# Optimization experiments

Hardware: AMD Instinct MI355X
Metric: run time of the kernel (lower is better)

Reference implementation:

```python
import jax, jax.numpy as jnp
import numpy as np

B, C, H = 64, 64, 32

def _pm_cross_pairs(ks):
    # Replicates PM_cross(2, ks): pairs (i, i+j) ordered by gap j=1..ks-1, then i.
    a, b = [], []
    for j in range(1, ks):
        for i in range(ks - j):
            a.append(i)
            b.append(i + j)
    return np.array(a, dtype=np.int32), np.array(b, dtype=np.int32)

def setup_inputs() -> dict:
    key = jax.random.key(0)
    k1, k2 = jax.random.split(key)
    ia, ib = _pm_cross_pairs(H)           # 496 pairs for H=32
    hk = ia.shape[0] + 2 * H              # 560
    x = jax.random.normal(k1, (B, C, H, H), dtype=jnp.float32)
    weight = 0.1 * jax.random.normal(k2, (C, H, hk, H), dtype=jnp.float32)
    return {"x": x, "weight": weight, "idx_a": jnp.asarray(ia), "idx_b": jnp.asarray(ib)}

def reference(x, weight, idx_a, idx_b):
    # cross-term products along last axis: [B,C,H,P]
    cross = x[..., idx_a] * x[..., idx_b]
    feat = jnp.concatenate([x, x * x, cross], axis=-1)  # [B,C,H,Hk]
    # per-(channel,row) grouped matmul
    return jnp.einsum('bcij,cijo->bcio', feat, weight)
```

## Files before the change

kernel.cpp:

```cpp
#include <hip/hip_runtime.h>

#define NB 64
#define NC 64
#define NH 32
#define HK 560
#define NOCT 88
#define NCHUNK 11
#define XSTR 50

typedef __bf16 bf16x8 __attribute__((ext_vector_type(8)));
typedef float f32x4 __attribute__((ext_vector_type(4)));

__global__ __launch_bounds__(256, 4) void hconv_kernel(
    const float* __restrict__ x, const float* __restrict__ w,
    const int* __restrict__ idx_a, const int* __restrict__ idx_b,
    float* __restrict__ out)
{
    __shared__ float s_x[NB * XSTR];
    __shared__ unsigned s_desc[NOCT];
    __shared__ __align__(16) unsigned short s_wT[2][32][72];

    const int t = threadIdx.x;
    const int g = blockIdx.x;
    const int c = g >> 5, i = g & 31;

    {
        const int xrow = t >> 2, seg = t & 3;
        const float* xr = x + (((size_t)xrow * NC + c) * NH + i) * NH + seg * 8;
        float4 v0 = *(const float4*)(xr);
        float4 v1 = *(const float4*)(xr + 4);
        float* dst = &s_x[xrow * XSTR + seg * 8];
        dst[0] = v0.x; dst[1] = v0.y; dst[2] = v0.z; dst[3] = v0.w;
        dst[4] = v1.x; dst[5] = v1.y; dst[6] = v1.z; dst[7] = v1.w;
        if (seg == 0) {
            #pragma unroll
            for (int m = 0; m < 8; ++m) {
                s_x[xrow * XSTR + 32 + m] = 0.0f;
                s_x[xrow * XSTR + 40 + m] = 1.0f;
            }
        }
    }

    if (t < NOCT) {
        unsigned pa, pb, ko, val;
        if (t < 4)      { pa = 8u * t; pb = 40u; ko = 8u * t; val = 8u; }
        else if (t < 8) { unsigned u = t - 4; pa = pb = 8u * u; ko = 32u + 8u * u; val = 8u; }
        else if (t < 84) {
            unsigned q = t - 8, j, a;
            if (q < 28)      { j = 1 + q / 4;        a = q % 4; }
            else if (q < 52) { j = 8 + (q - 28) / 3; a = (q - 28) % 3; }
            else if (q < 68) { j = 16 + (q - 52) / 2; a = (q - 52) % 2; }
            else             { j = 24 + (q - 68);     a = 0; }
            unsigned r = 32 - j;
            pa = 8 * a; pb = 8 * a + j;
            unsigned rem = r - 8 * a;
            val = rem < 8u ? rem : 8u;
            ko = 64u + (j - 1) * 32u - (j * (j - 1)) / 2u + 8u * a;
        } else { pa = 40u; pb = 40u; ko = 0u; val = 0u; }
        s_desc[t] = pa | (pb << 6) | (ko << 12) | (val << 22);
    }

    const int wv = t >> 6;
    const int lane = t & 63;
    const int lr = lane & 15;
    const int lq = lane >> 4;
    const int arow = wv * 16 + lr;
    const int wo = t & 31;
    const int wkg = t >> 5;

    const float* wbase = w + (size_t)(c * NH + i) * HK * NH;

    __syncthreads();

    {
        const unsigned d = s_desc[wkg];
        const unsigned ko = (d >> 12) & 0x3ffu, val = d >> 22;
        bf16x8 wv8;
        #pragma unroll
        for (int r = 0; r < 8; ++r) {
            float v = (r < (int)val)
                ? __builtin_nontemporal_load(&wbase[(size_t)(ko + r) * NH + wo]) : 0.0f;
            wv8[r] = (__bf16)v;
        }
        *(bf16x8*)&s_wT[0][wo][wkg * 8] = wv8;
    }
    __syncthreads();

    f32x4 acc0 = {0.f, 0.f, 0.f, 0.f};
    f32x4 acc1 = {0.f, 0.f, 0.f, 0.f};

    for (int ch = 0; ch < NCHUNK; ++ch) {
        const int buf = ch & 1;

        float pv[8];
        if (ch + 1 < NCHUNK) {
            const unsigned d = s_desc[(ch + 1) * 8 + wkg];
            const unsigned ko = (d >> 12) & 0x3ffu, val = d >> 22;
            #pragma unroll
            for (int r = 0; r < 8; ++r)
                pv[r] = (r < (int)val)
                    ? __builtin_nontemporal_load(&wbase[(size_t)(ko + r) * NH + wo]) : 0.0f;
        }

        #pragma unroll
        for (int ks = 0; ks < 2; ++ks) {
            const unsigned d = s_desc[ch * 8 + ks * 4 + lq];
            const float* pA = &s_x[arow * XSTR + (d & 63u)];
            const float* pB = &s_x[arow * XSTR + ((d >> 6) & 63u)];
            bf16x8 a;
            #pragma unroll
            for (int j2 = 0; j2 < 8; ++j2)
                a[j2] = (__bf16)(pA[j2] * pB[j2]);
            bf16x8 b0 = *(const bf16x8*)&s_wT[buf][lr][ks * 32 + lq * 8];
            bf16x8 b1 = *(const bf16x8*)&s_wT[buf][16 + lr][ks * 32 + lq * 8];
            acc0 = __builtin_amdgcn_mfma_f32_16x16x32_bf16(a, b0, acc0, 0, 0, 0);
            acc1 = __builtin_amdgcn_mfma_f32_16x16x32_bf16(a, b1, acc1, 0, 0, 0);
        }

        if (ch + 1 < NCHUNK) {
            bf16x8 wv8;
            #pragma unroll
            for (int r = 0; r < 8; ++r) wv8[r] = (__bf16)pv[r];
            *(bf16x8*)&s_wT[buf ^ 1][wo][wkg * 8] = wv8;
        }
        __syncthreads();
    }

    #pragma unroll
    for (int r = 0; r < 4; ++r) {
        const int b = wv * 16 + lq * 4 + r;
        float* op = out + (((size_t)b * NC + c) * NH + i) * NH;
        op[lr] = acc0[r];
        op[16 + lr] = acc1[r];
    }
}

extern "C" void kernel_launch(void* const* d_in, const int* in_sizes, int n_in,
                              void* d_out, int out_size, void* d_ws, size_t ws_size,
                              hipStream_t stream) {
    const float* x = (const float*)d_in[0];
    const float* w = (const float*)d_in[1];
    const int* idx_a = (const int*)d_in[2];
    const int* idx_b = (const int*)d_in[3];
    float* out = (float*)d_out;
    hconv_kernel<<<dim3(NC * NH), dim3(256), 0, stream>>>(x, w, idx_a, idx_b, out);
}
```

Measured before the change: 278.6 us.

## Load weights directly into registers per wave, dropping LDS staging and barriers

Removes the shared-memory weight staging buffer and its per-chunk __syncthreads. Each wave now loads its B-fragment weights straight from global memory into registers and converts them to bf16. Partial final octets are handled by clamping ko to 552 and shifting the x offsets, with zero padding in a wider x row (stride 57), so the per-row valid-count masking is no longer needed. This raises the occupancy hint to 5 blocks per CU. The trade-off is that the four waves each load the same weights redundantly, relying on the cache, and the loads no longer use nontemporal hints.

```diff
diff --git a/kernel.cpp b/kernel.cpp
--- a/kernel.cpp
+++ b/kernel.cpp
@@ -6,19 +6,18 @@
 #define HK 560
 #define NOCT 88
 #define NCHUNK 11
-#define XSTR 50
+#define XSTR 57
 
 typedef __bf16 bf16x8 __attribute__((ext_vector_type(8)));
 typedef float f32x4 __attribute__((ext_vector_type(4)));
 
-__global__ __launch_bounds__(256, 4) void hconv_kernel(
+__global__ __launch_bounds__(256, 5) void hconv_kernel(
     const float* __restrict__ x, const float* __restrict__ w,
     const int* __restrict__ idx_a, const int* __restrict__ idx_b,
     float* __restrict__ out)
 {
     __shared__ float s_x[NB * XSTR];
     __shared__ unsigned s_desc[NOCT];
-    __shared__ __align__(16) unsigned short s_wT[2][32][72];
 
     const int t = threadIdx.x;
     const int g = blockIdx.x;
@@ -29,101 +28,93 @@
         const float* xr = x + (((size_t)xrow * NC + c) * NH + i) * NH + seg * 8;
         float4 v0 = *(const float4*)(xr);
         float4 v1 = *(const float4*)(xr + 4);
-        float* dst = &s_x[xrow * XSTR + seg * 8];
+        float* dst = &s_x[xrow * XSTR + 8 + seg * 8];
         dst[0] = v0.x; dst[1] = v0.y; dst[2] = v0.z; dst[3] = v0.w;
         dst[4] = v1.x; dst[5] = v1.y; dst[6] = v1.z; dst[7] = v1.w;
         if (seg == 0) {
+            float* r0 = &s_x[xrow * XSTR];
             #pragma unroll
             for (int m = 0; m < 8; ++m) {
-                s_x[xrow * XSTR + 32 + m] = 0.0f;
-                s_x[xrow * XSTR + 40 + m] = 1.0f;
+                r0[m] = 0.0f;
+                r0[40 + m] = 0.0f;
+                r0[48 + m] = 1.0f;
             }
         }
     }
 
     if (t < NOCT) {
-        unsigned pa, pb, ko, val;
-        if (t < 4)      { pa = 8u * t; pb = 40u; ko = 8u * t; val = 8u; }
-        else if (t < 8) { unsigned u = t - 4; pa = pb = 8u * u; ko = 32u + 8u * u; val = 8u; }
+        unsigned pa, pb, ko;
+        if (t < 4)      { pa = 8u + 8u * t; pb = 48u; ko = 8u * t; }
+        else if (t < 8) { unsigned u = t - 4; pa = pb = 8u + 8u * u; ko = 32u + 8u * u; }
         else if (t < 84) {
             unsigned q = t - 8, j, a;
-            if (q < 28)      { j = 1 + q / 4;        a = q % 4; }
-            else if (q < 52) { j = 8 + (q - 28) / 3; a = (q - 28) % 3; }
+            if (q < 28)      { j = 1 + q / 4;         a = q % 4; }
+            else if (q < 52) { j = 8 + (q - 28) / 3;  a = (q - 28) % 3; }
             else if (q < 68) { j = 16 + (q - 52) / 2; a = (q - 52) % 2; }
             else             { j = 24 + (q - 68);     a = 0; }
-            unsigned r = 32 - j;
-            pa = 8 * a; pb = 8 * a + j;
-            unsigned rem = r - 8 * a;
-            val = rem < 8u ? rem : 8u;
             ko = 64u + (j - 1) * 32u - (j * (j - 1)) / 2u + 8u * a;
-        } else { pa = 40u; pb = 40u; ko = 0u; val = 0u; }
-        s_desc[t] = pa | (pb << 6) | (ko << 12) | (val << 22);
+            pa = 8u + 8u * a; pb = pa + j;
+            if (ko > 552u) { unsigned s = ko - 552u; ko = 552u; pa -= s; pb -= s; }
+        } else { pa = 0u; pb = 0u; ko = 0u; }
+        s_desc[t] = pa | (pb << 6) | (ko << 12);
     }
 
-    const int wv = t >> 6;
-    const int lane = t & 63;
-    const int lr = lane & 15;
-    const int lq = lane >> 4;
+    const int wv = t >> 6, lane = t & 63;
+    const int lr = lane & 15, lq = lane >> 4;
     const int arow = wv * 16 + lr;
-    const int wo = t & 31;
-    const int wkg = t >> 5;
+    const float* wbase = w + (size_t)(c * NH + i) * HK * NH;
+    const float* xrp = &s_x[arow * XSTR];
 
-    const float* wbase = w + (size_t)(c * NH + i) * HK * NH;
-
-    __syncthreads();
-
-    {
-        const unsigned d = s_desc[wkg];
-        const unsigned ko = (d >> 12) & 0x3ffu, val = d >> 22;
-        bf16x8 wv8;
-        #pragma unroll
-        for (int r = 0; r < 8; ++r) {
-            float v = (r < (int)val)
-                ? __builtin_nontemporal_load(&wbase[(size_t)(ko + r) * NH + wo]) : 0.0f;
-            wv8[r] = (__bf16)v;
-        }
-        *(bf16x8*)&s_wT[0][wo][wkg * 8] = wv8;
-    }
     __syncthreads();
 
     f32x4 acc0 = {0.f, 0.f, 0.f, 0.f};
     f32x4 acc1 = {0.f, 0.f, 0.f, 0.f};
 
+    unsigned d0 = s_desc[lq];
+    unsigned d1 = s_desc[4 + lq];
+
     for (int ch = 0; ch < NCHUNK; ++ch) {
-        const int buf = ch & 1;
+        unsigned nd0 = 0, nd1 = 0;
+        if (ch + 1 < NCHUNK) {
+            nd0 = s_desc[(ch + 1) * 8 + lq];
+            nd1 = s_desc[(ch + 1) * 8 + 4 + lq];
+        }
+        const unsigned pa0 = d0 & 63u, pb0 = (d0 >> 6) & 63u, ko0 = d0 >> 12;
+        const unsigned pa1 = d1 & 63u, pb1 = (d1 >> 6) & 63u, ko1 = d1 >> 12;
 
-        float pv[8];
-        if (ch + 1 < NCHUNK) {
-            const unsigned d = s_desc[(ch + 1) * 8 + wkg];
-            const unsigned ko = (d >> 12) & 0x3ffu, val = d >> 22;
-            #pragma unroll
-            for (int r = 0; r < 8; ++r)
-                pv[r] = (r < (int)val)
-                    ? __builtin_nontemporal_load(&wbase[(size_t)(ko + r) * NH + wo]) : 0.0f;
+        const float* wb0 = wbase + (size_t)ko0 * NH + lr;
+        const float* wb1 = wbase + (size_t)ko1 * NH + lr;
+        float b0v[8], b1v[8], b2v[8], b3v[8];
+        #pragma unroll
+        for (int j = 0; j < 8; ++j) {
+            b0v[j] = wb0[j * NH];
+            b1v[j] = wb0[j * NH + 16];
+            b2v[j] = wb1[j * NH];
+            b3v[j] = wb1[j * NH + 16];
         }
 
+        const float* pA0 = xrp + pa0; const float* pB0 = xrp + pb0;
+        const float* pA1 = xrp + pa1; const float* pB1 = xrp + pb1;
+        bf16x8 a0, a1;
         #pragma unroll
-        for (int ks = 0; ks < 2; ++ks) {
-            const unsigned d = s_desc[ch * 8 + ks * 4 + lq];
-            const float* pA = &s_x[arow * XSTR + (d & 63u)];
-            const float* pB = &s_x[arow * XSTR + ((d >> 6) & 63u)];
-            bf16x8 a;
-            #pragma unroll
-            for (int j2 = 0; j2 < 8; ++j2)
-                a[j2] = (__bf16)(pA[j2] * pB[j2]);
-            bf16x8 b0 = *(const bf16x8*)&s_wT[buf][lr][ks * 32 + lq * 8];
-            bf16x8 b1 = *(const bf16x8*)&s_wT[buf][16 + lr][ks * 32 + lq * 8];
-            acc0 = __builtin_amdgcn_mfma_f32_16x16x32_bf16(a, b0, acc0, 0, 0, 0);
-            acc1 = __builtin_amdgcn_mfma_f32_16x16x32_bf16(a, b1, acc1, 0, 0, 0);
+        for (int j = 0; j < 8; ++j) {
+            a0[j] = (__bf16)(pA0[j] * pB0[j]);
+            a1[j] = (__bf16)(pA1[j] * pB1[j]);
         }
 
-        if (ch + 1 < NCHUNK) {
-            bf16x8 wv8;
-            #pragma unroll
-            for (int r = 0; r < 8; ++r) wv8[r] = (__bf16)pv[r];
-            *(bf16x8*)&s_wT[buf ^ 1][wo][wkg * 8] = wv8;
+        bf16x8 f0, f1, f2, f3;
+        #pragma unroll
+        for (int j = 0; j < 8; ++j) {
+            f0[j] = (__bf16)b0v[j]; f1[j] = (__bf16)b1v[j];
+            f2[j] = (__bf16)b2v[j]; f3[j] = (__bf16)b3v[j];
         }
-        __syncthreads();
+
+        acc0 = __builtin_amdgcn_mfma_f32_16x16x32_bf16(a0, f0, acc0, 0, 0, 0);
+        acc1 = __builtin_amdgcn_mfma_f32_16x16x32_bf16(a0, f1, acc1, 0, 0, 0);
+        acc0 = __builtin_amdgcn_mfma_f32_16x16x32_bf16(a1, f2, acc0, 0, 0, 0);
+        acc1 = __builtin_amdgcn_mfma_f32_16x16x32_bf16(a1, f3, acc1, 0, 0, 0);
+
+        d0 = nd0; d1 = nd1;
     }
 
     #pragma unroll
```

Result: faster. 240.8 us (-13.6%).
